# Kernel optimization log

Hardware: AMD Instinct MI355X
Metric: run time of the kernel (lower is better)

Reference implementation:

```python
import jax, jax.numpy as jnp
import numpy as np

B = 1048576

def _mlp3(x, W1, b1, W2, b2, W3, b3):
    # x: [..., d] -> [..., 1]; Linear(d,d)+ReLU, Linear(d,d)+ReLU, Linear(d,1)
    h = jax.nn.relu(jnp.einsum('...d,od->...o', x, W1) + b1)
    h = jax.nn.relu(jnp.einsum('...d,od->...o', h, W2) + b2)
    return jnp.einsum('...d,od->...o', h, W3) + b3

def setup_inputs() -> dict:
    key = jax.random.key(0)
    ks = jax.random.split(key, 20)
    def lin(k, out_d, in_d):
        bound = 1.0 / np.sqrt(in_d)
        k1, k2 = jax.random.split(k)
        W = jax.random.uniform(k1, (out_d, in_d), jnp.float32, -bound, bound)
        b = jax.random.uniform(k2, (out_d,), jnp.float32, -bound, bound)
        return W, b
    inp = {
        'edge': jax.random.normal(ks[0], (B, 4, 10), jnp.float32),
        'cross': jax.random.normal(ks[1], (B, 4, 8), jnp.float32),
        'corner': jax.random.normal(ks[2], (B, 4, 10), jnp.float32),
        'cn': jax.random.normal(ks[3], (B, 1), jnp.float32),
    }
    eW1, eb1 = lin(ks[4], 10, 10); eW2, eb2 = lin(ks[5], 10, 10); eW3, eb3 = lin(ks[6], 1, 10)
    xW1, xb1 = lin(ks[7], 8, 8);  xW2, xb2 = lin(ks[8], 8, 8);  xW3, xb3 = lin(ks[9], 1, 8)
    cW1, cb1 = lin(ks[10], 10, 10); cW2, cb2 = lin(ks[11], 10, 10); cW3, cb3 = lin(ks[12], 1, 10)
    nW, nb = lin(ks[13], 1, 1)
    inp.update(dict(eW1=eW1, eb1=eb1, eW2=eW2, eb2=eb2, eW3=eW3, eb3=eb3,
                    xW1=xW1, xb1=xb1, xW2=xW2, xb2=xb2, xW3=xW3, xb3=xb3,
                    cW1=cW1, cb1=cb1, cW2=cW2, cb2=cb2, cW3=cW3, cb3=cb3,
                    nW=nW, nb=nb))
    return inp

def reference(edge, cross, corner, cn,
              eW1, eb1, eW2, eb2, eW3, eb3,
              xW1, xb1, xW2, xb2, xW3, xb3,
              cW1, cb1, cW2, cb2, cW3, cb3,
              nW, nb) -> jnp.ndarray:
    # Shared-weight MLP over each of the 4 slices, summed over the slice dim.
    e = _mlp3(edge, eW1, eb1, eW2, eb2, eW3, eb3).sum(axis=1)    # [B,1]
    x = _mlp3(cross, xW1, xb1, xW2, xb2, xW3, xb3).sum(axis=1)   # [B,1]
    c = _mlp3(corner, cW1, cb1, cW2, cb2, cW3, cb3).sum(axis=1)  # [B,1]
    n = jnp.einsum('bd,od->bo', cn, nW) + nb                     # [B,1]
    return e + x + c + n
```

## Files before the change

### kernel.cpp

```cpp
#include <hip/hip_runtime.h>


typedef float f2 __attribute__((ext_vector_type(2)));

template<int F4, int PSTR>
__device__ __forceinline__ void stage(const float* __restrict__ in,
                                      float* __restrict__ sm, int t, int blk)
{
    const float4* src = reinterpret_cast<const float4*>(in) + (size_t)blk * (256 * F4);
    #pragma unroll
    for (int it = 0; it < F4; ++it) {
        const int g = it * 256 + t;
        float4 v = src[g];
        const int e = g / F4;
        const int j = g - e * F4;
        *reinterpret_cast<float4*>(sm + e * PSTR + j * 4) = v;
    }
}

template<int D>
__device__ __forceinline__ float mlp4(const float* __restrict__ xl,
                                      const float* __restrict__ W1,
                                      const float* __restrict__ b1,
                                      const float* __restrict__ W2,
                                      const float* __restrict__ b2,
                                      const float* __restrict__ W3,
                                      const float* __restrict__ b3)
{
    constexpr int H = D / 2;
    f2 oacc = {0.0f, 0.0f};
    #pragma unroll
    for (int s = 0; s < 4; ++s) {
        f2 xs[H];
        #pragma unroll
        for (int k = 0; k < H; ++k)
            xs[k] = *reinterpret_cast<const f2*>(xl + s * D + 2 * k);

        f2 h1[H];
        #pragma unroll
        for (int op = 0; op < H; ++op) {
            f2 a = {b1[2 * op], b1[2 * op + 1]};
            #pragma unroll
            for (int i = 0; i < D; ++i) {
                const float xv = (i & 1) ? xs[i >> 1].y : xs[i >> 1].x;
                const f2 w = {W1[(2 * op) * D + i], W1[(2 * op + 1) * D + i]};
                a = __builtin_elementwise_fma(w, (f2){xv, xv}, a);
            }
            h1[op] = __builtin_elementwise_max(a, (f2){0.0f, 0.0f});
        }

        f2 h2[H];
        #pragma unroll
        for (int op = 0; op < H; ++op) {
            f2 a = {b2[2 * op], b2[2 * op + 1]};
            #pragma unroll
            for (int i = 0; i < D; ++i) {
                const float hv = (i & 1) ? h1[i >> 1].y : h1[i >> 1].x;
                const f2 w = {W2[(2 * op) * D + i], W2[(2 * op + 1) * D + i]};
                a = __builtin_elementwise_fma(w, (f2){hv, hv}, a);
            }
            h2[op] = __builtin_elementwise_max(a, (f2){0.0f, 0.0f});
        }

        #pragma unroll
        for (int k = 0; k < H; ++k) {
            const f2 w3 = {W3[2 * k], W3[2 * k + 1]};
            oacc = __builtin_elementwise_fma(w3, h2[k], oacc);
        }
    }
    return oacc.x + oacc.y + 4.0f * b3[0];
}

__global__ __launch_bounds__(256)
void osero_kernel(const float* __restrict__ edge,
                  const float* __restrict__ cross_,
                  const float* __restrict__ corner,
                  const float* __restrict__ cn,
                  const float* __restrict__ eW1, const float* __restrict__ eb1,
                  const float* __restrict__ eW2, const float* __restrict__ eb2,
                  const float* __restrict__ eW3, const float* __restrict__ eb3,
                  const float* __restrict__ xW1, const float* __restrict__ xb1,
                  const float* __restrict__ xW2, const float* __restrict__ xb2,
                  const float* __restrict__ xW3, const float* __restrict__ xb3,
                  const float* __restrict__ cW1, const float* __restrict__ cb1,
                  const float* __restrict__ cW2, const float* __restrict__ cb2,
                  const float* __restrict__ cW3, const float* __restrict__ cb3,
                  const float* __restrict__ nW,  const float* __restrict__ nb,
                  float* __restrict__ out)
{
    __shared__ __align__(16) float sm[256 * 44];

    const int t   = threadIdx.x;
    const int blk = blockIdx.x;
    const int y   = blockIdx.y;
    const int b   = blk * 256 + t;

    float val;
    if (y == 0) {
        stage<10, 44>(edge, sm, t, blk);
        __syncthreads();
        val = mlp4<10>(sm + t * 44, eW1, eb1, eW2, eb2, eW3, eb3);
    } else if (y == 1) {
        stage<10, 44>(corner, sm, t, blk);
        __syncthreads();
        val = mlp4<10>(sm + t * 44, cW1, cb1, cW2, cb2, cW3, cb3);
    } else {
        stage<8, 36>(cross_, sm, t, blk);
        __syncthreads();
        val = mlp4<8>(sm + t * 36, xW1, xb1, xW2, xb2, xW3, xb3);
        val += fmaf(cn[b], nW[0], nb[0]);
    }

    unsafeAtomicAdd(out + b, val);
}

extern "C" void kernel_launch(void* const* d_in, const int* in_sizes, int n_in,
                              void* d_out, int out_size, void* d_ws, size_t ws_size,
                              hipStream_t stream) {
    const float* edge   = (const float*)d_in[0];
    const float* cross_ = (const float*)d_in[1];
    const float* corner = (const float*)d_in[2];
    const float* cn     = (const float*)d_in[3];
    const float* eW1 = (const float*)d_in[4];
    const float* eb1 = (const float*)d_in[5];
    const float* eW2 = (const float*)d_in[6];
    const float* eb2 = (const float*)d_in[7];
    const float* eW3 = (const float*)d_in[8];
    const float* eb3 = (const float*)d_in[9];
    const float* xW1 = (const float*)d_in[10];
    const float* xb1 = (const float*)d_in[11];
    const float* xW2 = (const float*)d_in[12];
    const float* xb2 = (const float*)d_in[13];
    const float* xW3 = (const float*)d_in[14];
    const float* xb3 = (const float*)d_in[15];
    const float* cW1 = (const float*)d_in[16];
    const float* cb1 = (const float*)d_in[17];
    const float* cW2 = (const float*)d_in[18];
    const float* cb2 = (const float*)d_in[19];
    const float* cW3 = (const float*)d_in[20];
    const float* cb3 = (const float*)d_in[21];
    const float* nW  = (const float*)d_in[22];
    const float* nb  = (const float*)d_in[23];

    const int nelem = in_sizes[3];
    const int nblk  = (nelem + 255) / 256;

    hipMemsetAsync(d_out, 0, (size_t)out_size * sizeof(float), stream);

    dim3 grid(nblk, 3);
    osero_kernel<<<grid, 256, 0, stream>>>(edge, cross_, corner, cn,
                                           eW1, eb1, eW2, eb2, eW3, eb3,
                                           xW1, xb1, xW2, xb2, xW3, xb3,
                                           cW1, cb1, cW2, cb2, cW3, cb3,
                                           nW, nb, (float*)d_out);
}
```

Measured before the change: 450.0 us.

## Map one thread per slice, fuse all three MLPs, reduce with shuffles

The work is remapped so each thread handles one (element, slice) pair and evaluates the edge, corner and cross MLPs together, loading its inputs straight from global memory with no shared-memory staging or barrier. The four slices of an element are summed with quad shuffles and written once with a plain store. This removes the memset, the atomic adds and the 3-way grid split. The cost is four times as many threads, per-thread strided vector loads in place of coalesced float4 staging, and three MLPs' worth of register use in one thread.

After: 460.1 us. 2.2% more time.

```diff
diff --git a/kernel.cpp b/kernel.cpp
--- a/kernel.cpp
+++ b/kernel.cpp
@@ -3,72 +3,50 @@
 
 typedef float f2 __attribute__((ext_vector_type(2)));
 
-template<int F4, int PSTR>
-__device__ __forceinline__ void stage(const float* __restrict__ in,
-                                      float* __restrict__ sm, int t, int blk)
-{
-    const float4* src = reinterpret_cast<const float4*>(in) + (size_t)blk * (256 * F4);
-    #pragma unroll
-    for (int it = 0; it < F4; ++it) {
-        const int g = it * 256 + t;
-        float4 v = src[g];
-        const int e = g / F4;
-        const int j = g - e * F4;
-        *reinterpret_cast<float4*>(sm + e * PSTR + j * 4) = v;
-    }
-}
-
 template<int D>
-__device__ __forceinline__ float mlp4(const float* __restrict__ xl,
-                                      const float* __restrict__ W1,
-                                      const float* __restrict__ b1,
-                                      const float* __restrict__ W2,
-                                      const float* __restrict__ b2,
-                                      const float* __restrict__ W3,
-                                      const float* __restrict__ b3)
+__device__ __forceinline__ float mlp_slice(const f2* xs,
+                                           const float* __restrict__ W1,
+                                           const float* __restrict__ b1,
+                                           const float* __restrict__ W2,
+                                           const float* __restrict__ b2,
+                                           const float* __restrict__ W3,
+                                           const float* __restrict__ b3)
 {
     constexpr int H = D / 2;
-    f2 oacc = {0.0f, 0.0f};
+
+    f2 h1[H];
     #pragma unroll
-    for (int s = 0; s < 4; ++s) {
-        f2 xs[H];
+    for (int op = 0; op < H; ++op) {
+        f2 a = {b1[2 * op], b1[2 * op + 1]};
         #pragma unroll
-        for (int k = 0; k < H; ++k)
-            xs[k] = *reinterpret_cast<const f2*>(xl + s * D + 2 * k);
+        for (int i = 0; i < D; ++i) {
+            const float xv = (i & 1) ? xs[i >> 1].y : xs[i >> 1].x;
+            const f2 w = {W1[(2 * op) * D + i], W1[(2 * op + 1) * D + i]};
+            a = __builtin_elementwise_fma(w, (f2){xv, xv}, a);
+        }
+        h1[op] = __builtin_elementwise_max(a, (f2){0.0f, 0.0f});
+    }
 
-        f2 h1[H];
+    f2 h2[H];
+    #pragma unroll
+    for (int op = 0; op < H; ++op) {
+        f2 a = {b2[2 * op], b2[2 * op + 1]};
         #pragma unroll
-        for (int op = 0; op < H; ++op) {
-            f2 a = {b1[2 * op], b1[2 * op + 1]};
-            #pragma unroll
-            for (int i = 0; i < D; ++i) {
-                const float xv = (i & 1) ? xs[i >> 1].y : xs[i >> 1].x;
-                const f2 w = {W1[(2 * op) * D + i], W1[(2 * op + 1) * D + i]};
-                a = __builtin_elementwise_fma(w, (f2){xv, xv}, a);
-            }
-            h1[op] = __builtin_elementwise_max(a, (f2){0.0f, 0.0f});
+        for (int i = 0; i < D; ++i) {
+            const float hv = (i & 1) ? h1[i >> 1].y : h1[i >> 1].x;
+            const f2 w = {W2[(2 * op) * D + i], W2[(2 * op + 1) * D + i]};
+            a = __builtin_elementwise_fma(w, (f2){hv, hv}, a);
         }
+        h2[op] = __builtin_elementwise_max(a, (f2){0.0f, 0.0f});
+    }
 
-        f2 h2[H];
-        #pragma unroll
-        for (int op = 0; op < H; ++op) {
-            f2 a = {b2[2 * op], b2[2 * op + 1]};
-            #pragma unroll
-            for (int i = 0; i < D; ++i) {
-                const float hv = (i & 1) ? h1[i >> 1].y : h1[i >> 1].x;
-                const f2 w = {W2[(2 * op) * D + i], W2[(2 * op + 1) * D + i]};
-                a = __builtin_elementwise_fma(w, (f2){hv, hv}, a);
-            }
-            h2[op] = __builtin_elementwise_max(a, (f2){0.0f, 0.0f});
-        }
-
-        #pragma unroll
-        for (int k = 0; k < H; ++k) {
-            const f2 w3 = {W3[2 * k], W3[2 * k + 1]};
-            oacc = __builtin_elementwise_fma(w3, h2[k], oacc);
-        }
+    f2 o = {0.0f, 0.0f};
+    #pragma unroll
+    for (int k = 0; k < H; ++k) {
+        const f2 w3 = {W3[2 * k], W3[2 * k + 1]};
+        o = __builtin_elementwise_fma(w3, h2[k], o);
     }
-    return oacc.x + oacc.y + 4.0f * b3[0];
+    return o.x + o.y + b3[0];
 }
 
 __global__ __launch_bounds__(256)
@@ -86,32 +64,44 @@
                   const float* __restrict__ cW2, const float* __restrict__ cb2,
                   const float* __restrict__ cW3, const float* __restrict__ cb3,
                   const float* __restrict__ nW,  const float* __restrict__ nb,
-                  float* __restrict__ out)
+                  float* __restrict__ out, int nelem)
 {
-    __shared__ __align__(16) float sm[256 * 44];
+    const int g = blockIdx.x * 256 + threadIdx.x;
+    const int e = g >> 2;
+    const int s = g & 3;
+    if (e >= nelem) return;
 
-    const int t   = threadIdx.x;
-    const int blk = blockIdx.x;
-    const int y   = blockIdx.y;
-    const int b   = blk * 256 + t;
+    f2 xe[5];
+    {
+        const f2* p = reinterpret_cast<const f2*>(edge) + (size_t)g * 5;
+        #pragma unroll
+        for (int k = 0; k < 5; ++k) xe[k] = p[k];
+    }
+    f2 xq[5];
+    {
+        const f2* p = reinterpret_cast<const f2*>(corner) + (size_t)g * 5;
+        #pragma unroll
+        for (int k = 0; k < 5; ++k) xq[k] = p[k];
+    }
+    f2 xc[4];
+    {
+        const float4* p = reinterpret_cast<const float4*>(cross_) + (size_t)g * 2;
+        const float4 v0 = p[0];
+        const float4 v1 = p[1];
+        xc[0] = (f2){v0.x, v0.y}; xc[1] = (f2){v0.z, v0.w};
+        xc[2] = (f2){v1.x, v1.y}; xc[3] = (f2){v1.z, v1.w};
+    }
+    const float cnv = (s == 0) ? cn[e] : 0.0f;
 
-    float val;
-    if (y == 0) {
-        stage<10, 44>(edge, sm, t, blk);
-        __syncthreads();
-        val = mlp4<10>(sm + t * 44, eW1, eb1, eW2, eb2, eW3, eb3);
-    } else if (y == 1) {
-        stage<10, 44>(corner, sm, t, blk);
-        __syncthreads();
-        val = mlp4<10>(sm + t * 44, cW1, cb1, cW2, cb2, cW3, cb3);
-    } else {
-        stage<8, 36>(cross_, sm, t, blk);
-        __syncthreads();
-        val = mlp4<8>(sm + t * 36, xW1, xb1, xW2, xb2, xW3, xb3);
-        val += fmaf(cn[b], nW[0], nb[0]);
-    }
+    float val = mlp_slice<10>(xe, eW1, eb1, eW2, eb2, eW3, eb3);
+    val      += mlp_slice<10>(xq, cW1, cb1, cW2, cb2, cW3, cb3);
+    val      += mlp_slice<8> (xc, xW1, xb1, xW2, xb2, xW3, xb3);
 
-    unsafeAtomicAdd(out + b, val);
+    val += __shfl_xor(val, 1, 4);
+    val += __shfl_xor(val, 2, 4);
+
+    if (s == 0)
+        out[e] = val + fmaf(cnv, nW[0], nb[0]);
 }
 
 extern "C" void kernel_launch(void* const* d_in, const int* in_sizes, int n_in,
@@ -143,14 +133,12 @@
     const float* nb  = (const float*)d_in[23];
 
     const int nelem = in_sizes[3];
-    const int nblk  = (nelem + 255) / 256;
+    const int nthr  = nelem * 4;
+    const int nblk  = (nthr + 255) / 256;
 
-    hipMemsetAsync(d_out, 0, (size_t)out_size * sizeof(float), stream);
-
-    dim3 grid(nblk, 3);
-    osero_kernel<<<grid, 256, 0, stream>>>(edge, cross_, corner, cn,
-                                           eW1, eb1, eW2, eb2, eW3, eb3,
-                                           xW1, xb1, xW2, xb2, xW3, xb3,
-                                           cW1, cb1, cW2, cb2, cW3, cb3,
-                                           nW, nb, (float*)d_out);
+    osero_kernel<<<dim3(nblk), 256, 0, stream>>>(edge, cross_, corner, cn,
+                                                 eW1, eb1, eW2, eb2, eW3, eb3,
+                                                 xW1, xb1, xW2, xb2, xW3, xb3,
+                                                 cW1, cb1, cW2, cb2, cW3, cb3,
+                                                 nW, nb, (float*)d_out, nelem);
 }
```
